# Performance work log

Measured on AMD Instinct MI355X. Metric: run time of the kernel, lower is better.

The kernel has to match this reference:

```python
import jax, jax.numpy as jnp
import numpy as np

DIM_X, H1, H2 = 1024, 2048, 512
SL, SU = 8192, 16384
K_TRIES = 8  # vectorized stand-in for the per-sample rejection-sampling while-loop


def setup_inputs() -> dict:
    key = jax.random.key(0)
    ks = jax.random.split(key, 10)
    s = 0.02
    return {
        "X_l": jax.random.normal(ks[0], (SL, DIM_X), jnp.float32),
        "y_l": jax.random.normal(ks[1], (SL,), jnp.float32),
        "X_u": jax.random.normal(ks[2], (SU, DIM_X), jnp.float32),
        "y_u": jax.random.normal(ks[3], (SU,), jnp.float32),
        "W1": jax.random.normal(ks[4], (DIM_X, H1), jnp.float32) * s,
        "b1": jnp.zeros((H1,), jnp.float32),
        "W2": jax.random.normal(ks[5], (H1, H2), jnp.float32) * s,
        "b2": jnp.zeros((H2,), jnp.float32),
        "W3": jax.random.normal(ks[6], (H2, 1), jnp.float32) * s,
        "b3": jnp.zeros((1,), jnp.float32),
    }


def _sample_pairs(key, y_l, size_u):
    """For each unlabeled sample, draw a labeled pair (a, b) with a != b and
    y_l[a] != y_l[b] (mirrors torch.randperm + rejection loop). K candidate
    draws per sample; first valid candidate is taken (valid w.h.p. for
    continuous y_l)."""
    size_l = y_l.shape[0]
    ka, kb = jax.random.split(key)
    ia = jax.random.randint(ka, (size_u, K_TRIES), 0, size_l)  # [SU, K]
    ib = jax.random.randint(kb, (size_u, K_TRIES), 0, size_l)
    valid = (ia != ib) & (y_l[ia] != y_l[ib])
    first = jnp.argmax(valid, axis=1)  # first valid candidate per row
    a = jnp.take_along_axis(ia, first[:, None], axis=1)[:, 0]
    b = jnp.take_along_axis(ib, first[:, None], axis=1)[:, 0]
    return a, b


def reference(X_l, y_l, X_u, y_u, W1, b1, W2, b2, W3, b3):
    def encode(x):
        h = jax.nn.relu(x @ W1 + b1)
        return jax.nn.relu(h @ W2 + b2)

    feat_l = encode(X_l)          # [SL, H2]
    feat_u = encode(X_u)          # [SU, H2]
    y_hat = feat_l @ W3 + b3      # [SL, 1]

    a, b = _sample_pairs(jax.random.key(42), y_l, X_u.shape[0])
    k = (y_u - y_l[b]) / (y_l[a] - y_l[b])            # [SU]
    feat_comb = k[:, None] * feat_l[a] + (1.0 - k)[:, None] * feat_l[b]
    return feat_u, feat_comb, y_hat
```

## Files before the change

### kernel.cpp

```cpp
#include <hip/hip_runtime.h>
#include <stdint.h>

#define SLAB 8192
#define SUNL 16384
#define DIMX 1024
#define HID1 2048
#define HID2 512
#define KTRIES 8

typedef __attribute__((ext_vector_type(8))) short bf16x8;
typedef __attribute__((ext_vector_type(4))) float f32x4;

__device__ __forceinline__ unsigned short f2bf(float f) {
  union { float f; uint32_t u; } c; c.f = f;
  return (unsigned short)((c.u + 0x7fffu + ((c.u >> 16) & 1u)) >> 16);
}

__device__ __forceinline__ void async16(const void* g, void* l) {
  __builtin_amdgcn_global_load_lds(
      (const __attribute__((address_space(1))) unsigned int*)g,
      (__attribute__((address_space(3))) unsigned int*)l,
      16, 0, 0);
}

struct U2 { uint32_t x, y; };

__device__ __forceinline__ U2 threefry(uint32_t k0, uint32_t k1, uint32_t x0, uint32_t x1) {
  uint32_t ks2 = k0 ^ k1 ^ 0x1BD11BDAu;
  x0 += k0; x1 += k1;
#define TF_R(r) { x0 += x1; x1 = (x1 << (r)) | (x1 >> (32 - (r))); x1 ^= x0; }
  TF_R(13) TF_R(15) TF_R(26) TF_R(6)
  x0 += k1; x1 += ks2 + 1u;
  TF_R(17) TF_R(29) TF_R(16) TF_R(24)
  x0 += ks2; x1 += k0 + 2u;
  TF_R(13) TF_R(15) TF_R(26) TF_R(6)
  x0 += k0; x1 += k1 + 3u;
  TF_R(17) TF_R(29) TF_R(16) TF_R(24)
  x0 += k1; x1 += ks2 + 4u;
  TF_R(13) TF_R(15) TF_R(26) TF_R(6)
  x0 += ks2; x1 += k0 + 5u;
#undef TF_R
  return {x0, x1};
}

__global__ __launch_bounds__(256) void pairs_kernel(
    const float* __restrict__ y_l, const float* __restrict__ y_u,
    int* __restrict__ ai, int* __restrict__ bi, float* __restrict__ kv)
{
  int r = blockIdx.x * 256 + threadIdx.x;
  if (r >= SUNL) return;

  U2 ka  = threefry(0u, 42u, 0u, 0u);
  U2 kb  = threefry(0u, 42u, 0u, 1u);
  U2 k2a = threefry(ka.x, ka.y, 0u, 1u);
  U2 k2b = threefry(kb.x, kb.y, 0u, 1u);

  int iav[KTRIES], ibv[KTRIES];
#pragma unroll
  for (int c = 0; c < KTRIES; ++c) {
    uint32_t t = (uint32_t)(r * KTRIES + c);
    U2 oa = threefry(k2a.x, k2a.y, 0u, t);
    U2 ob = threefry(k2b.x, k2b.y, 0u, t);
    iav[c] = (int)((oa.x ^ oa.y) & (SLAB - 1));
    ibv[c] = (int)((ob.x ^ ob.y) & (SLAB - 1));
  }
  int a = iav[0], b = ibv[0];
#pragma unroll
  for (int c = 0; c < KTRIES; ++c) {
    if (iav[c] != ibv[c] && y_l[iav[c]] != y_l[ibv[c]]) { a = iav[c]; b = ibv[c]; break; }
  }
  float ya = y_l[a], yb = y_l[b];
  ai[r] = a; bi[r] = b; kv[r] = (y_u[r] - yb) / (ya - yb);
}

#define XL_BLOCKS (SLAB * DIMX / 4 / 256)
__global__ __launch_bounds__(256) void cast_bf16_kernel(
    const float* __restrict__ Xl, const float* __restrict__ Xu,
    unsigned short* __restrict__ Xb)
{
  size_t bi = blockIdx.x;
  const float* src; size_t i;
  if (bi < XL_BLOCKS) { src = Xl; i = bi * 256 + threadIdx.x; }
  else { src = Xu; i = (bi - XL_BLOCKS) * 256 + threadIdx.x; }
  float4 v = ((const float4*)src)[i];
  ushort4 o;
  o.x = f2bf(v.x); o.y = f2bf(v.y); o.z = f2bf(v.z); o.w = f2bf(v.w);
  size_t doff = (bi < XL_BLOCKS) ? 0 : (size_t)SLAB * DIMX / 4;
  ((ushort4*)Xb)[doff + i] = o;
}

__global__ void transpose_cast_kernel(
    const float* __restrict__ W, unsigned short* __restrict__ WT, int K, int N)
{
  __shared__ float t[32][33];
  int k0 = blockIdx.y * 32, n0 = blockIdx.x * 32;
  int tx = threadIdx.x, ty = threadIdx.y;
#pragma unroll
  for (int i = 0; i < 32; i += 8)
    t[ty + i][tx] = W[(size_t)(k0 + ty + i) * N + n0 + tx];
  __syncthreads();
#pragma unroll
  for (int i = 0; i < 32; i += 8)
    WT[(size_t)(n0 + ty + i) * K + k0 + tx] = f2bf(t[tx][ty + i]);
}

template<int OUT_BF16, int RELU>
__global__ __launch_bounds__(256) void gemm_bt_mfma(
    const unsigned short* __restrict__ A,
    const unsigned short* __restrict__ Bt,
    const float* __restrict__ bias,
    void* __restrict__ C0, void* __restrict__ C1, int Msplit,
    int M, int N, int K)
{
  __shared__ unsigned short As[128 * 32];
  __shared__ unsigned short Bs[128 * 32];

  const int tid  = threadIdx.x;
  const int wave = tid >> 6;
  const int lane = tid & 63;
  const int m0 = blockIdx.y * 128;
  const int n0 = blockIdx.x * 128;
  const int wm = (wave >> 1) * 64;
  const int wn = (wave & 1) * 64;

  const int srow  = wave * 32 + (lane >> 2);
  const int gchunk = ((lane & 3) - (srow >> 1)) & 3;
  const int scol  = gchunk * 8;
  const unsigned short* gA = A  + (size_t)(m0 + srow) * K + scol;
  const unsigned short* gB = Bt + (size_t)(n0 + srow) * K + scol;
  unsigned short* lA = As + wave * 32 * 32;
  unsigned short* lB = Bs + wave * 32 * 32;

  const int fr = lane & 15;
  const int q  = lane >> 4;

  f32x4 acc[4][4] = {};

  for (int k0 = 0; k0 < K; k0 += 32) {
    async16(gA + k0,                  lA);
    async16(gA + k0 + (size_t)16 * K, lA + 16 * 32);
    async16(gB + k0,                  lB);
    async16(gB + k0 + (size_t)16 * K, lB + 16 * 32);
    __syncthreads();

    bf16x8 ar[4], br[4];
#pragma unroll
    for (int i = 0; i < 4; ++i) {
      int rowA = wm + i * 16 + fr;
      int rowB = wn + i * 16 + fr;
      int slotA = ((q + (rowA >> 1)) & 3) * 8;
      int slotB = ((q + (rowB >> 1)) & 3) * 8;
      ar[i] = *(const bf16x8*)(As + rowA * 32 + slotA);
      br[i] = *(const bf16x8*)(Bs + rowB * 32 + slotB);
    }
#pragma unroll
    for (int i = 0; i < 4; ++i)
#pragma unroll
      for (int j = 0; j < 4; ++j)
        acc[i][j] = __builtin_amdgcn_mfma_f32_16x16x32_bf16(ar[i], br[j], acc[i][j], 0, 0, 0);
    __syncthreads();
  }

  void* Cb = (m0 < Msplit) ? C0 : C1;
  const int mbase = (m0 < Msplit) ? m0 : (m0 - Msplit);
  const int crow = mbase + wm + (lane >> 4) * 4;
  const int ccol = n0 + wn + (lane & 15);
#pragma unroll
  for (int j = 0; j < 4; ++j) {
    float bv = bias[ccol + j * 16];
#pragma unroll
    for (int i = 0; i < 4; ++i) {
#pragma unroll
      for (int r = 0; r < 4; ++r) {
        float v = acc[i][j][r] + bv;
        if (RELU) v = fmaxf(v, 0.0f);
        size_t idx = (size_t)(crow + i * 16 + r) * N + ccol + j * 16;
        if (OUT_BF16) ((unsigned short*)Cb)[idx] = f2bf(v);
        else          ((float*)Cb)[idx] = v;
      }
    }
  }
}

__global__ __launch_bounds__(256) void yhat_kernel(
    const float* __restrict__ feat_l, const float* __restrict__ W3,
    const float* __restrict__ b3, float* __restrict__ out)
{
  int wave = threadIdx.x >> 6;
  int lane = threadIdx.x & 63;
  int row = blockIdx.x * 4 + wave;
  if (row >= SLAB) return;
  const float* f = feat_l + (size_t)row * HID2;
  float s = 0.f;
#pragma unroll
  for (int j = 0; j < HID2 / 64; ++j) s = fmaf(f[lane + j * 64], W3[lane + j * 64], s);
#pragma unroll
  for (int off = 32; off; off >>= 1) s += __shfl_down(s, off);
  if (lane == 0) out[row] = s + b3[0];
}

__global__ __launch_bounds__(256) void comb_kernel(
    const float* __restrict__ feat_l, const int* __restrict__ ai,
    const int* __restrict__ bi, const float* __restrict__ kv,
    float* __restrict__ out)
{
  int row = blockIdx.x * 2 + (threadIdx.x >> 7);
  int c = (threadIdx.x & 127) << 2;
  float k = kv[row];
  float km1 = 1.0f - k;
  float4 fa = *(const float4*)(feat_l + (size_t)ai[row] * HID2 + c);
  float4 fb = *(const float4*)(feat_l + (size_t)bi[row] * HID2 + c);
  float4 o;
  o.x = k * fa.x + km1 * fb.x;
  o.y = k * fa.y + km1 * fb.y;
  o.z = k * fa.z + km1 * fb.z;
  o.w = k * fa.w + km1 * fb.w;
  *(float4*)(out + (size_t)row * HID2 + c) = o;
}

extern "C" void kernel_launch(void* const* d_in, const int* in_sizes, int n_in,
                              void* d_out, int out_size, void* d_ws, size_t ws_size,
                              hipStream_t stream)
{
  const float* X_l = (const float*)d_in[0];
  const float* y_l = (const float*)d_in[1];
  const float* X_u = (const float*)d_in[2];
  const float* y_u = (const float*)d_in[3];
  const float* W1  = (const float*)d_in[4];
  const float* b1  = (const float*)d_in[5];
  const float* W2  = (const float*)d_in[6];
  const float* b2  = (const float*)d_in[7];
  const float* W3  = (const float*)d_in[8];
  const float* b3  = (const float*)d_in[9];

  float* out_featu = (float*)d_out;
  float* out_comb  = out_featu + (size_t)SUNL * HID2;
  float* out_yhat  = out_comb + (size_t)SUNL * HID2;

  unsigned short* X_bf  = (unsigned short*)d_ws;
  unsigned short* W1T   = X_bf + (size_t)(SLAB + SUNL) * DIMX;
  unsigned short* W2T   = W1T + (size_t)HID1 * DIMX;
  unsigned short* H_bf  = W2T + (size_t)HID2 * HID1;
  float* feat_l = (float*)(H_bf + (size_t)(SLAB + SUNL) * HID1);
  int*   ai = (int*)(feat_l + (size_t)SLAB * HID2);
  int*   bi = ai + SUNL;
  float* kv = (float*)(bi + SUNL);

  const int MTOT = SLAB + SUNL;

  dim3 blk(256);
  dim3 tblk(32, 8);

  pairs_kernel<<<dim3(SUNL / 256), blk, 0, stream>>>(y_l, y_u, ai, bi, kv);

  cast_bf16_kernel<<<dim3(MTOT * DIMX / 4 / 256), blk, 0, stream>>>(X_l, X_u, X_bf);
  transpose_cast_kernel<<<dim3(HID1 / 32, DIMX / 32), tblk, 0, stream>>>(W1, W1T, DIMX, HID1);
  transpose_cast_kernel<<<dim3(HID2 / 32, HID1 / 32), tblk, 0, stream>>>(W2, W2T, HID1, HID2);

  gemm_bt_mfma<1, 1><<<dim3(HID1 / 128, MTOT / 128), blk, 0, stream>>>(
      X_bf, W1T, b1, H_bf, H_bf, MTOT * 2 , MTOT, HID1, DIMX);

  gemm_bt_mfma<0, 1><<<dim3(HID2 / 128, MTOT / 128), blk, 0, stream>>>(
      H_bf, W2T, b2, feat_l, out_featu, SLAB, MTOT, HID2, HID1);

  yhat_kernel<<<dim3(SLAB / 4), blk, 0, stream>>>(feat_l, W3, b3, out_yhat);
  comb_kernel<<<dim3(SUNL / 2), blk, 0, stream>>>(feat_l, ai, bi, kv, out_comb);
}
```

Measured before the change: 390.6 us.

## Merge prep and post kernels, switch GEMM to 32x32 MFMA with grouped tile order

Merges the cast, both weight transposes and the pair sampling into a single prep launch, and merges the comb and y_hat kernels into a single post launch, cutting launch count from eight to four. The GEMM now uses 32x32x16 bf16 MFMA instructions instead of 16x16x32, with a 2x2 accumulator grid per wave. Its block index is remapped to a grouped M-major order (GROUP_M=8) for better L2 reuse of B tiles. Risks are different LDS read patterns and a strided epilogue store layout, and the branchy merged kernels may add divergence overhead.

```diff
diff --git a/kernel.cpp b/kernel.cpp
--- a/kernel.cpp
+++ b/kernel.cpp
@@ -7,9 +7,11 @@
 #define HID1 2048
 #define HID2 512
 #define KTRIES 8
+#define MTOT (SLAB + SUNL)
 
 typedef __attribute__((ext_vector_type(8))) short bf16x8;
 typedef __attribute__((ext_vector_type(4))) float f32x4;
+typedef __attribute__((ext_vector_type(16))) float f32x16;
 
 __device__ __forceinline__ unsigned short f2bf(float f) {
   union { float f; uint32_t u; } c; c.f = f;
@@ -43,66 +45,79 @@
   return {x0, x1};
 }
 
-__global__ __launch_bounds__(256) void pairs_kernel(
+#define XL_BLOCKS (SLAB * DIMX / 4 / 256)
+#define CAST_BLOCKS (MTOT * DIMX / 4 / 256)
+#define T1_NBX (HID1 / 32)
+#define T1_BLOCKS ((HID1 / 32) * (DIMX / 32))
+#define T2_NBX (HID2 / 32)
+#define T2_BLOCKS ((HID2 / 32) * (HID1 / 32))
+#define PAIR_BLOCKS (SUNL / 256)
+#define PREP_BLOCKS (CAST_BLOCKS + T1_BLOCKS + T2_BLOCKS + PAIR_BLOCKS)
+
+__global__ __launch_bounds__(256) void prep_kernel(
+    const float* __restrict__ Xl, const float* __restrict__ Xu,
+    const float* __restrict__ W1, const float* __restrict__ W2,
     const float* __restrict__ y_l, const float* __restrict__ y_u,
-    int* __restrict__ ai, int* __restrict__ bi, float* __restrict__ kv)
-{
-  int r = blockIdx.x * 256 + threadIdx.x;
-  if (r >= SUNL) return;
-
-  U2 ka  = threefry(0u, 42u, 0u, 0u);
-  U2 kb  = threefry(0u, 42u, 0u, 1u);
-  U2 k2a = threefry(ka.x, ka.y, 0u, 1u);
-  U2 k2b = threefry(kb.x, kb.y, 0u, 1u);
-
-  int iav[KTRIES], ibv[KTRIES];
-#pragma unroll
-  for (int c = 0; c < KTRIES; ++c) {
-    uint32_t t = (uint32_t)(r * KTRIES + c);
-    U2 oa = threefry(k2a.x, k2a.y, 0u, t);
-    U2 ob = threefry(k2b.x, k2b.y, 0u, t);
-    iav[c] = (int)((oa.x ^ oa.y) & (SLAB - 1));
-    ibv[c] = (int)((ob.x ^ ob.y) & (SLAB - 1));
-  }
-  int a = iav[0], b = ibv[0];
-#pragma unroll
-  for (int c = 0; c < KTRIES; ++c) {
-    if (iav[c] != ibv[c] && y_l[iav[c]] != y_l[ibv[c]]) { a = iav[c]; b = ibv[c]; break; }
-  }
-  float ya = y_l[a], yb = y_l[b];
-  ai[r] = a; bi[r] = b; kv[r] = (y_u[r] - yb) / (ya - yb);
-}
-
-#define XL_BLOCKS (SLAB * DIMX / 4 / 256)
-__global__ __launch_bounds__(256) void cast_bf16_kernel(
-    const float* __restrict__ Xl, const float* __restrict__ Xu,
-    unsigned short* __restrict__ Xb)
-{
-  size_t bi = blockIdx.x;
-  const float* src; size_t i;
-  if (bi < XL_BLOCKS) { src = Xl; i = bi * 256 + threadIdx.x; }
-  else { src = Xu; i = (bi - XL_BLOCKS) * 256 + threadIdx.x; }
-  float4 v = ((const float4*)src)[i];
-  ushort4 o;
-  o.x = f2bf(v.x); o.y = f2bf(v.y); o.z = f2bf(v.z); o.w = f2bf(v.w);
-  size_t doff = (bi < XL_BLOCKS) ? 0 : (size_t)SLAB * DIMX / 4;
-  ((ushort4*)Xb)[doff + i] = o;
-}
-
-__global__ void transpose_cast_kernel(
-    const float* __restrict__ W, unsigned short* __restrict__ WT, int K, int N)
+    unsigned short* __restrict__ X_bf, unsigned short* __restrict__ W1T,
+    unsigned short* __restrict__ W2T,
+    int* __restrict__ ia, int* __restrict__ ib, float* __restrict__ kv)
 {
   __shared__ float t[32][33];
-  int k0 = blockIdx.y * 32, n0 = blockIdx.x * 32;
-  int tx = threadIdx.x, ty = threadIdx.y;
-#pragma unroll
-  for (int i = 0; i < 32; i += 8)
-    t[ty + i][tx] = W[(size_t)(k0 + ty + i) * N + n0 + tx];
-  __syncthreads();
-#pragma unroll
-  for (int i = 0; i < 32; i += 8)
-    WT[(size_t)(n0 + ty + i) * K + k0 + tx] = f2bf(t[tx][ty + i]);
-}
+  int b = blockIdx.x;
+  int tid = threadIdx.x;
+
+  if (b < CAST_BLOCKS) {
+    const float* src; size_t i, doff;
+    if (b < XL_BLOCKS) { src = Xl; i = (size_t)b * 256 + tid; doff = 0; }
+    else { src = Xu; i = (size_t)(b - XL_BLOCKS) * 256 + tid; doff = (size_t)SLAB * DIMX / 4; }
+    float4 v = ((const float4*)src)[i];
+    ushort4 o;
+    o.x = f2bf(v.x); o.y = f2bf(v.y); o.z = f2bf(v.z); o.w = f2bf(v.w);
+    ((ushort4*)X_bf)[doff + i] = o;
+  } else if (b < CAST_BLOCKS + T1_BLOCKS + T2_BLOCKS) {
+    const float* W; unsigned short* WT; int K, N, bx, by;
+    if (b < CAST_BLOCKS + T1_BLOCKS) {
+      int tb = b - CAST_BLOCKS;
+      W = W1; WT = W1T; K = DIMX; N = HID1; bx = tb % T1_NBX; by = tb / T1_NBX;
+    } else {
+      int tb = b - CAST_BLOCKS - T1_BLOCKS;
+      W = W2; WT = W2T; K = HID1; N = HID2; bx = tb % T2_NBX; by = tb / T2_NBX;
+    }
+    int k0 = by * 32, n0 = bx * 32;
+    int tx = tid & 31, ty = tid >> 5;
+#pragma unroll
+    for (int i = 0; i < 32; i += 8)
+      t[ty + i][tx] = W[(size_t)(k0 + ty + i) * N + n0 + tx];
+    __syncthreads();
+#pragma unroll
+    for (int i = 0; i < 32; i += 8)
+      WT[(size_t)(n0 + ty + i) * K + k0 + tx] = f2bf(t[tx][ty + i]);
+  } else {
+    int r = (b - CAST_BLOCKS - T1_BLOCKS - T2_BLOCKS) * 256 + tid;
+    U2 ka  = threefry(0u, 42u, 0u, 0u);
+    U2 kb  = threefry(0u, 42u, 0u, 1u);
+    U2 k2a = threefry(ka.x, ka.y, 0u, 1u);
+    U2 k2b = threefry(kb.x, kb.y, 0u, 1u);
+    int iav[KTRIES], ibv[KTRIES];
+#pragma unroll
+    for (int c = 0; c < KTRIES; ++c) {
+      uint32_t tt = (uint32_t)(r * KTRIES + c);
+      U2 oa = threefry(k2a.x, k2a.y, 0u, tt);
+      U2 ob = threefry(k2b.x, k2b.y, 0u, tt);
+      iav[c] = (int)((oa.x ^ oa.y) & (SLAB - 1));
+      ibv[c] = (int)((ob.x ^ ob.y) & (SLAB - 1));
+    }
+    int a = iav[0], bb2 = ibv[0];
+#pragma unroll
+    for (int c = 0; c < KTRIES; ++c) {
+      if (iav[c] != ibv[c] && y_l[iav[c]] != y_l[ibv[c]]) { a = iav[c]; bb2 = ibv[c]; break; }
+    }
+    float ya = y_l[a], yb = y_l[bb2];
+    ia[r] = a; ib[r] = bb2; kv[r] = (y_u[r] - yb) / (ya - yb);
+  }
+}
+
+#define GROUP_M 8
 
 template<int OUT_BF16, int RELU>
 __global__ __launch_bounds__(256) void gemm_bt_mfma(
@@ -118,23 +133,27 @@
   const int tid  = threadIdx.x;
   const int wave = tid >> 6;
   const int lane = tid & 63;
-  const int m0 = blockIdx.y * 128;
-  const int n0 = blockIdx.x * 128;
+
+  const int nbx = N / 128;
+  const int gsize = nbx * GROUP_M;
+  const int grp = blockIdx.x / gsize, within = blockIdx.x % gsize;
+  const int m0 = (grp * GROUP_M + (within % GROUP_M)) * 128;
+  const int n0 = (within / GROUP_M) * 128;
+
   const int wm = (wave >> 1) * 64;
   const int wn = (wave & 1) * 64;
 
   const int srow  = wave * 32 + (lane >> 2);
   const int gchunk = ((lane & 3) - (srow >> 1)) & 3;
-  const int scol  = gchunk * 8;
-  const unsigned short* gA = A  + (size_t)(m0 + srow) * K + scol;
-  const unsigned short* gB = Bt + (size_t)(n0 + srow) * K + scol;
+  const unsigned short* gA = A  + (size_t)(m0 + srow) * K + gchunk * 8;
+  const unsigned short* gB = Bt + (size_t)(n0 + srow) * K + gchunk * 8;
   unsigned short* lA = As + wave * 32 * 32;
   unsigned short* lB = Bs + wave * 32 * 32;
 
-  const int fr = lane & 15;
-  const int q  = lane >> 4;
-
-  f32x4 acc[4][4] = {};
+  const int r31 = lane & 31;
+  const int cHalf = lane >> 5;
+
+  f32x16 acc[2][2] = {};
 
   for (int k0 = 0; k0 < K; k0 += 32) {
     async16(gA + k0,                  lA);
@@ -143,38 +162,43 @@
     async16(gB + k0 + (size_t)16 * K, lB + 16 * 32);
     __syncthreads();
 
-    bf16x8 ar[4], br[4];
-#pragma unroll
-    for (int i = 0; i < 4; ++i) {
-      int rowA = wm + i * 16 + fr;
-      int rowB = wn + i * 16 + fr;
-      int slotA = ((q + (rowA >> 1)) & 3) * 8;
-      int slotB = ((q + (rowB >> 1)) & 3) * 8;
-      ar[i] = *(const bf16x8*)(As + rowA * 32 + slotA);
-      br[i] = *(const bf16x8*)(Bs + rowB * 32 + slotB);
-    }
-#pragma unroll
-    for (int i = 0; i < 4; ++i)
-#pragma unroll
-      for (int j = 0; j < 4; ++j)
-        acc[i][j] = __builtin_amdgcn_mfma_f32_16x16x32_bf16(ar[i], br[j], acc[i][j], 0, 0, 0);
+    bf16x8 ar[2][2], br[2][2];
+#pragma unroll
+    for (int i = 0; i < 2; ++i) {
+      int rowA = wm + i * 32 + r31;
+      int rowB = wn + i * 32 + r31;
+#pragma unroll
+      for (int kk = 0; kk < 2; ++kk) {
+        int c = kk * 2 + cHalf;
+        ar[i][kk] = *(const bf16x8*)(As + rowA * 32 + ((c + (rowA >> 1)) & 3) * 8);
+        br[i][kk] = *(const bf16x8*)(Bs + rowB * 32 + ((c + (rowB >> 1)) & 3) * 8);
+      }
+    }
+#pragma unroll
+    for (int kk = 0; kk < 2; ++kk)
+#pragma unroll
+      for (int i = 0; i < 2; ++i)
+#pragma unroll
+        for (int j = 0; j < 2; ++j)
+          acc[i][j] = __builtin_amdgcn_mfma_f32_32x32x16_bf16(ar[i][kk], br[j][kk], acc[i][j], 0, 0, 0);
     __syncthreads();
   }
 
   void* Cb = (m0 < Msplit) ? C0 : C1;
-  const int mbase = (m0 < Msplit) ? m0 : (m0 - Msplit);
-  const int crow = mbase + wm + (lane >> 4) * 4;
-  const int ccol = n0 + wn + (lane & 15);
-#pragma unroll
-  for (int j = 0; j < 4; ++j) {
-    float bv = bias[ccol + j * 16];
-#pragma unroll
-    for (int i = 0; i < 4; ++i) {
-#pragma unroll
-      for (int r = 0; r < 4; ++r) {
-        float v = acc[i][j][r] + bv;
+  const int mbase = ((m0 < Msplit) ? m0 : (m0 - Msplit)) + wm;
+  const int ccolBase = n0 + wn + (lane & 31);
+  const int crowHi = (lane >> 5) * 4;
+#pragma unroll
+  for (int j = 0; j < 2; ++j) {
+    float bv = bias[ccolBase + j * 32];
+#pragma unroll
+    for (int i = 0; i < 2; ++i) {
+#pragma unroll
+      for (int reg = 0; reg < 16; ++reg) {
+        int row = (reg & 3) + 8 * (reg >> 2) + crowHi;
+        float v = acc[i][j][reg] + bv;
         if (RELU) v = fmaxf(v, 0.0f);
-        size_t idx = (size_t)(crow + i * 16 + r) * N + ccol + j * 16;
+        size_t idx = (size_t)(mbase + i * 32 + row) * N + ccolBase + j * 32;
         if (OUT_BF16) ((unsigned short*)Cb)[idx] = f2bf(v);
         else          ((float*)Cb)[idx] = v;
       }
@@ -182,40 +206,42 @@
   }
 }
 
-__global__ __launch_bounds__(256) void yhat_kernel(
+#define COMB_BLOCKS (SUNL / 2)
+#define YHAT_BLOCKS (SLAB / 4)
+#define POST_BLOCKS (COMB_BLOCKS + YHAT_BLOCKS)
+
+__global__ __launch_bounds__(256) void post_kernel(
     const float* __restrict__ feat_l, const float* __restrict__ W3,
-    const float* __restrict__ b3, float* __restrict__ out)
-{
-  int wave = threadIdx.x >> 6;
-  int lane = threadIdx.x & 63;
-  int row = blockIdx.x * 4 + wave;
-  if (row >= SLAB) return;
-  const float* f = feat_l + (size_t)row * HID2;
-  float s = 0.f;
-#pragma unroll
-  for (int j = 0; j < HID2 / 64; ++j) s = fmaf(f[lane + j * 64], W3[lane + j * 64], s);
-#pragma unroll
-  for (int off = 32; off; off >>= 1) s += __shfl_down(s, off);
-  if (lane == 0) out[row] = s + b3[0];
-}
-
-__global__ __launch_bounds__(256) void comb_kernel(
-    const float* __restrict__ feat_l, const int* __restrict__ ai,
-    const int* __restrict__ bi, const float* __restrict__ kv,
-    float* __restrict__ out)
-{
-  int row = blockIdx.x * 2 + (threadIdx.x >> 7);
-  int c = (threadIdx.x & 127) << 2;
-  float k = kv[row];
-  float km1 = 1.0f - k;
-  float4 fa = *(const float4*)(feat_l + (size_t)ai[row] * HID2 + c);
-  float4 fb = *(const float4*)(feat_l + (size_t)bi[row] * HID2 + c);
-  float4 o;
-  o.x = k * fa.x + km1 * fb.x;
-  o.y = k * fa.y + km1 * fb.y;
-  o.z = k * fa.z + km1 * fb.z;
-  o.w = k * fa.w + km1 * fb.w;
-  *(float4*)(out + (size_t)row * HID2 + c) = o;
+    const float* __restrict__ b3, const int* __restrict__ ia,
+    const int* __restrict__ ib, const float* __restrict__ kv,
+    float* __restrict__ out_comb, float* __restrict__ out_yhat)
+{
+  int b = blockIdx.x;
+  if (b < COMB_BLOCKS) {
+    int row = b * 2 + (threadIdx.x >> 7);
+    int c = (threadIdx.x & 127) << 2;
+    float k = kv[row];
+    float km1 = 1.0f - k;
+    float4 fa = *(const float4*)(feat_l + (size_t)ia[row] * HID2 + c);
+    float4 fb = *(const float4*)(feat_l + (size_t)ib[row] * HID2 + c);
+    float4 o;
+    o.x = k * fa.x + km1 * fb.x;
+    o.y = k * fa.y + km1 * fb.y;
+    o.z = k * fa.z + km1 * fb.z;
+    o.w = k * fa.w + km1 * fb.w;
+    *(float4*)(out_comb + (size_t)row * HID2 + c) = o;
+  } else {
+    int wave = threadIdx.x >> 6;
+    int lane = threadIdx.x & 63;
+    int row = (b - COMB_BLOCKS) * 4 + wave;
+    const float* f = feat_l + (size_t)row * HID2;
+    float s = 0.f;
+#pragma unroll
+    for (int j = 0; j < HID2 / 64; ++j) s = fmaf(f[lane + j * 64], W3[lane + j * 64], s);
+#pragma unroll
+    for (int off = 32; off; off >>= 1) s += __shfl_down(s, off);
+    if (lane == 0) out_yhat[row] = s + b3[0];
+  }
 }
 
 extern "C" void kernel_launch(void* const* d_in, const int* in_sizes, int n_in,
@@ -238,31 +264,25 @@
   float* out_yhat  = out_comb + (size_t)SUNL * HID2;
 
   unsigned short* X_bf  = (unsigned short*)d_ws;
-  unsigned short* W1T   = X_bf + (size_t)(SLAB + SUNL) * DIMX;
+  unsigned short* W1T   = X_bf + (size_t)MTOT * DIMX;
   unsigned short* W2T   = W1T + (size_t)HID1 * DIMX;
   unsigned short* H_bf  = W2T + (size_t)HID2 * HID1;
-  float* feat_l = (float*)(H_bf + (size_t)(SLAB + SUNL) * HID1);
+  float* feat_l = (float*)(H_bf + (size_t)MTOT * HID1);
   int*   ai = (int*)(feat_l + (size_t)SLAB * HID2);
   int*   bi = ai + SUNL;
   float* kv = (float*)(bi + SUNL);
 
-  const int MTOT = SLAB + SUNL;
-
   dim3 blk(256);
-  dim3 tblk(32, 8);
-
-  pairs_kernel<<<dim3(SUNL / 256), blk, 0, stream>>>(y_l, y_u, ai, bi, kv);
-
-  cast_bf16_kernel<<<dim3(MTOT * DIMX / 4 / 256), blk, 0, stream>>>(X_l, X_u, X_bf);
-  transpose_cast_kernel<<<dim3(HID1 / 32, DIMX / 32), tblk, 0, stream>>>(W1, W1T, DIMX, HID1);
-  transpose_cast_kernel<<<dim3(HID2 / 32, HID1 / 32), tblk, 0, stream>>>(W2, W2T, HID1, HID2);
-
-  gemm_bt_mfma<1, 1><<<dim3(HID1 / 128, MTOT / 128), blk, 0, stream>>>(
+
+  prep_kernel<<<dim3(PREP_BLOCKS), blk, 0, stream>>>(
+      X_l, X_u, W1, W2, y_l, y_u, X_bf, W1T, W2T, ai, bi, kv);
+
+  gemm_bt_mfma<1, 1><<<dim3((HID1 / 128) * (MTOT / 128)), blk, 0, stream>>>(
       X_bf, W1T, b1, H_bf, H_bf, MTOT * 2 , MTOT, HID1, DIMX);
 
-  gemm_bt_mfma<0, 1><<<dim3(HID2 / 128, MTOT / 128), blk, 0, stream>>>(
+  gemm_bt_mfma<0, 1><<<dim3((HID2 / 128) * (MTOT / 128)), blk, 0, stream>>>(
       H_bf, W2T, b2, feat_l, out_featu, SLAB, MTOT, HID2, HID1);
 
-  yhat_kernel<<<dim3(SLAB / 4), blk, 0, stream>>>(feat_l, W3, b3, out_yhat);
-  comb_kernel<<<dim3(SUNL / 2), blk, 0, stream>>>(feat_l, ai, bi, kv, out_comb);
-}
+  post_kernel<<<dim3(POST_BLOCKS), blk, 0, stream>>>(
+      feat_l, W3, b3, ai, bi, kv, out_comb, out_yhat);
+}
```

Measured after the change: 391.0 us. No clear change (+0.1%).
